# Kernel optimization log

Measured on AMD Instinct MI355X. Metric: run time of the kernel, lower is better.

## Reference

```python
import jax, jax.numpy as jnp
import numpy as np

B, T, N, D = 32, 32, 64, 512
H, OUT = 64, 256


def setup_inputs() -> dict:
    key = jax.random.key(0)
    ks = jax.random.split(key, 7)
    return {
        "inputs": jax.random.normal(ks[0], (B, T, N, D), dtype=jnp.float32),
        "ue_w": jax.random.normal(ks[1], (H, D), dtype=jnp.float32) * (1.0 / np.sqrt(D)),
        "ue_b": jax.random.normal(ks[2], (H,), dtype=jnp.float32) * 0.02,
        "be": jnp.zeros((H,), dtype=jnp.float32),
        "w_w": jax.random.normal(ks[3], (1, H), dtype=jnp.float32) * (1.0 / np.sqrt(H)),
        "w_b": jax.random.normal(ks[4], (1,), dtype=jnp.float32) * 0.02,
        "fc1_w": jax.random.normal(ks[5], (OUT, D), dtype=jnp.float32) * (1.0 / np.sqrt(D)),
        "fc1_b": jax.random.normal(ks[6], (OUT,), dtype=jnp.float32) * 0.02,
    }


def reference(inputs, ue_w, ue_b, be, w_w, w_b, fc1_w, fc1_b):
    # Train path of STAttn.
    b, t, n, d = inputs.shape
    x = inputs.reshape(b * t, n, d)                       # flatten(start=0, end=1)
    h = jnp.einsum('bnd,hd->bnh', x, ue_w) + ue_b + be    # ue(x) + be
    h = jax.nn.leaky_relu(h, negative_slope=0.2)
    e = jnp.einsum('bnh,oh->bno', h, w_w) + w_b           # [BT, N, 1] scores
    a = jax.nn.softmax(e, axis=-2)                        # softmax over N
    attr = jnp.sum(a * x, axis=1)                         # weighted pooling -> [BT, D]
    fc = attr @ fc1_w.T + fc1_b                           # [BT, 256]
    return fc.reshape(b, t, fc.shape[-1]).transpose(1, 0, 2)  # [T, B, 256]
```

## Files before the change

### kernel.cpp

```cpp
#include <hip/hip_runtime.h>


typedef __attribute__((ext_vector_type(8)))  short bf16x8;
typedef __attribute__((ext_vector_type(16))) float f32x16;

#define AS3(p) ((__attribute__((address_space(3))) void*)(p))
#define AS1(p) ((const __attribute__((address_space(1))) void*)(p))
#define WAITVM0() asm volatile("s_waitcnt vmcnt(0)" ::: "memory")
#define SCHEDB()  __builtin_amdgcn_sched_barrier(0)

__device__ __forceinline__ void split8t(const float* __restrict__ v,
                                        bf16x8& h8, bf16x8& l8) {
#pragma unroll
    for (int i = 0; i < 8; ++i) {
        const unsigned u = __float_as_uint(v[i]);
        h8[i] = (short)(u >> 16);
        const float hf = __uint_as_float(u & 0xFFFF0000u);
        l8[i] = (short)(__float_as_uint(v[i] - hf) >> 16);
    }
}

template<int MODE>
__global__ __launch_bounds__(512, 4) void stattn_main(
    const float* __restrict__ inp,
    const float* __restrict__ ue_w,
    const float* __restrict__ ue_b,
    const float* __restrict__ be,
    const float* __restrict__ w_w,
    const float* __restrict__ fc1_w,
    const float* __restrict__ fc1_b,
    float* __restrict__ dst)
{
    __shared__ __align__(16) float xb[2][64 * 64];
    __shared__ __align__(16) float wb[2][64 * 64];
    __shared__ float ep_s[2][64];
    __shared__ float a_s[64];
    __shared__ __align__(16) float attr_s[512];

    const int tid = threadIdx.x;
    const int wv  = tid >> 6;
    const int l   = tid & 63;
    const int l31 = l & 31;
    const int hi5 = l >> 5;
    const int kh  = wv & 1;
    const int jh  = (wv >> 1) & 1;
    const int nh  = wv >> 2;
    const float* __restrict__ xg = inp + (size_t)blockIdx.x * (64 * 512);

    const int r_a  = wv * 8 + (l >> 4);
    const int r_b  = r_a + 4;
    const int cph  = (l & 15) >> 1;
    const int hfl  = l & 1;
    const int colA = (cph ^ (r_a & 7)) * 8 + hfl * 4;
    const int colB = (cph ^ (r_b & 7)) * 8 + hfl * 4;
    const float* __restrict__ gxa = xg   + r_a * 512 + colA;
    const float* __restrict__ gxb = xg   + r_b * 512 + colB;
    const float* __restrict__ gwa = ue_w + r_a * 512 + colA;
    const float* __restrict__ gwb = ue_w + r_b * 512 + colB;

#define STAGE(buf, kt) do {                                                          \
    __builtin_amdgcn_global_load_lds(AS1(gxa + (kt) * 64),                           \
        AS3((char*)&xb[buf][0] + (wv * 8) * 256), 16, 0, 0);                         \
    __builtin_amdgcn_global_load_lds(AS1(gxb + (kt) * 64),                           \
        AS3((char*)&xb[buf][0] + (wv * 8 + 4) * 256), 16, 0, 0);                     \
    __builtin_amdgcn_global_load_lds(AS1(gwa + (kt) * 64),                           \
        AS3((char*)&wb[buf][0] + (wv * 8) * 256), 16, 0, 0);                         \
    __builtin_amdgcn_global_load_lds(AS1(gwb + (kt) * 64),                           \
        AS3((char*)&wb[buf][0] + (wv * 8 + 4) * 256), 16, 0, 0);                     \
} while (0)

    f32x16 acc = {};
    STAGE(0, 0);

    const int arow = nh * 32 + l31;
    const int brow = jh * 32 + l31;

#pragma unroll
    for (int kt = 0; kt < 8; ++kt) {
        const int cur = kt & 1;
        WAITVM0();
        SCHEDB();
        __builtin_amdgcn_s_barrier();
        SCHEDB();
        if (kt < 7) STAGE(cur ^ 1, kt + 1);
        const float* __restrict__ xrow = &xb[cur][arow * 64];
        const float* __restrict__ wrow = &wb[cur][brow * 64];
#pragma unroll
        for (int s = 0; s < 2; ++s) {
            const int ck = kh * 4 + 2 * s + hi5;
            const int pa = (ck ^ (arow & 7)) * 8;
            const int pb = (ck ^ (brow & 7)) * 8;
            float av[8], bv[8];
            *reinterpret_cast<float4*>(&av[0]) = *reinterpret_cast<const float4*>(&xrow[pa]);
            *reinterpret_cast<float4*>(&av[4]) = *reinterpret_cast<const float4*>(&xrow[pa + 4]);
            *reinterpret_cast<float4*>(&bv[0]) = *reinterpret_cast<const float4*>(&wrow[pb]);
            *reinterpret_cast<float4*>(&bv[4]) = *reinterpret_cast<const float4*>(&wrow[pb + 4]);
            bf16x8 ah, al, bh, bl;
            split8t(av, ah, al);
            split8t(bv, bh, bl);
            acc = __builtin_amdgcn_mfma_f32_32x32x16_bf16(ah, bh, acc, 0, 0, 0);
            acc = __builtin_amdgcn_mfma_f32_32x32x16_bf16(al, bh, acc, 0, 0, 0);
            acc = __builtin_amdgcn_mfma_f32_32x32x16_bf16(ah, bl, acc, 0, 0, 0);
        }
    }

    __syncthreads();
    {
        float* hp = &xb[0][0];
        const int toff = (nh * 2 + jh) * 1024 + l;
        if (kh == 1) {
#pragma unroll
            for (int r = 0; r < 16; ++r) hp[toff + r * 64] = acc[r];
        }
        __syncthreads();
        if (kh == 0) {
#pragma unroll
            for (int r = 0; r < 16; ++r) acc[r] += hp[toff + r * 64];
            const int j = jh * 32 + l31;
            const float bias = ue_b[j] + be[j];
            const float ww   = w_w[j];
#pragma unroll
            for (int r = 0; r < 16; ++r) {
                float hv = acc[r] + bias;
                hv = hv > 0.f ? hv : 0.2f * hv;
                float p = hv * ww;
                p += __shfl_xor(p, 1);
                p += __shfl_xor(p, 2);
                p += __shfl_xor(p, 4);
                p += __shfl_xor(p, 8);
                p += __shfl_xor(p, 16);
                if (l31 == 0) {
                    const int nr = (r & 3) + 8 * (r >> 2) + 4 * hi5;
                    ep_s[jh][nh * 32 + nr] = p;
                }
            }
        }
    }
    __syncthreads();

    {
        const float v = ep_s[0][l] + ep_s[1][l];
        float mx = v;
#pragma unroll
        for (int off = 32; off >= 1; off >>= 1) mx = fmaxf(mx, __shfl_xor(mx, off));
        const float ex = expf(v - mx);
        float sm = ex;
#pragma unroll
        for (int off = 32; off >= 1; off >>= 1) sm += __shfl_xor(sm, off);
        if (wv == 0) a_s[l] = ex / sm;
    }
    __syncthreads();

    {
        const int d = tid;
        float s = 0.f;
#pragma unroll 8
        for (int n = 0; n < 64; ++n) s = fmaf(a_s[n], xg[n * 512 + d], s);
        if (MODE == 0) {
            dst[(size_t)blockIdx.x * 512 + d] = s;
        } else {
            attr_s[d] = s;
        }
    }

    if (MODE == 1) {
        __syncthreads();
        const int o  = tid >> 1;
        const int ks = tid & 1;
        const float* __restrict__ wr = fc1_w + o * 512 + ks * 256;
        const float* __restrict__ ap = attr_s + ks * 256;
        float s0 = 0.f, s1 = 0.f, s2 = 0.f, s3 = 0.f;
#pragma unroll 8
        for (int i = 0; i < 64; ++i) {
            const float4 w4 = *reinterpret_cast<const float4*>(&wr[i * 4]);
            const float4 a4 = *reinterpret_cast<const float4*>(&ap[i * 4]);
            s0 = fmaf(a4.x, w4.x, s0);
            s1 = fmaf(a4.y, w4.y, s1);
            s2 = fmaf(a4.z, w4.z, s2);
            s3 = fmaf(a4.w, w4.w, s3);
        }
        float p = (s0 + s1) + (s2 + s3);
        p += __shfl_xor(p, 1);
        if (ks == 0) {
            const int bt  = blockIdx.x;
            const int row = (bt & 31) * 32 + (bt >> 5);
            dst[row * 256 + o] = p + fc1_b[o];
        }
    }
#undef STAGE
}

__global__ __launch_bounds__(256, 2) void stattn_fc2(
    const float* __restrict__ attr,
    const float* __restrict__ fc1_w,
    const float* __restrict__ fc1_b,
    float* __restrict__ out)
{
    __shared__ __align__(16) float at[32][516];
    const int tid = threadIdx.x;
    const int bm  = blockIdx.x;
    const int bn  = blockIdx.y;

    {
        const int row = tid >> 3;
        const int seg = tid & 7;
        const float* __restrict__ src = attr + (size_t)(bm * 32 + row) * 512 + seg * 64;
#pragma unroll
        for (int q = 0; q < 16; ++q)
            *reinterpret_cast<float4*>(&at[row][seg * 64 + q * 4]) =
                *reinterpret_cast<const float4*>(&src[q * 4]);
    }
    __syncthreads();

    const int tx = tid & 31;
    const int ty = tid >> 5;
    const int o  = bn * 32 + tx;
    const float* __restrict__ wr = fc1_w + (size_t)o * 512;
    float s0 = 0.f, s1 = 0.f, s2 = 0.f, s3 = 0.f;
#pragma unroll 4
    for (int kq = 0; kq < 128; ++kq) {
        const float4 w4 = *reinterpret_cast<const float4*>(&wr[kq * 4]);
        const float4 a0 = *reinterpret_cast<const float4*>(&at[ty * 4 + 0][kq * 4]);
        const float4 a1 = *reinterpret_cast<const float4*>(&at[ty * 4 + 1][kq * 4]);
        const float4 a2 = *reinterpret_cast<const float4*>(&at[ty * 4 + 2][kq * 4]);
        const float4 a3 = *reinterpret_cast<const float4*>(&at[ty * 4 + 3][kq * 4]);
        s0 += a0.x * w4.x + a0.y * w4.y + a0.z * w4.z + a0.w * w4.w;
        s1 += a1.x * w4.x + a1.y * w4.y + a1.z * w4.z + a1.w * w4.w;
        s2 += a2.x * w4.x + a2.y * w4.y + a2.z * w4.z + a2.w * w4.w;
        s3 += a3.x * w4.x + a3.y * w4.y + a3.z * w4.z + a3.w * w4.w;
    }
    const float fb = fc1_b[o];
    float sv[4] = {s0, s1, s2, s3};
#pragma unroll
    for (int j = 0; j < 4; ++j) {
        const int bt  = bm * 32 + ty * 4 + j;
        const int row = (bt & 31) * 32 + (bt >> 5);
        out[row * 256 + o] = sv[j] + fb;
    }
}

extern "C" void kernel_launch(void* const* d_in, const int* in_sizes, int n_in,
                              void* d_out, int out_size, void* d_ws, size_t ws_size,
                              hipStream_t stream) {
    const float* inp   = (const float*)d_in[0];
    const float* ue_w  = (const float*)d_in[1];
    const float* ue_b  = (const float*)d_in[2];
    const float* be    = (const float*)d_in[3];
    const float* w_w   = (const float*)d_in[4];
    const float* fc1_w = (const float*)d_in[6];
    const float* fc1_b = (const float*)d_in[7];
    float* out = (float*)d_out;

    const bool split = ws_size >= (size_t)1024 * 512 * 4;
    if (split) {
        float* attr = (float*)d_ws;
        stattn_main<0><<<1024, 512, 0, stream>>>(inp, ue_w, ue_b, be, w_w,
                                                 fc1_w, fc1_b, attr);
        stattn_fc2<<<dim3(32, 8), 256, 0, stream>>>(attr, fc1_w, fc1_b, out);
    } else {
        stattn_main<1><<<1024, 512, 0, stream>>>(inp, ue_w, ue_b, be, w_w,
                                                 fc1_w, fc1_b, out);
    }
}
```

Baseline: 74.30 us.

## Process two tokens per block with direct global MFMA operand loads, drop LDS staging

Each 512-thread block now handles two BT slices. Each group of four waves computes a full-K 64x64 score tile, reading MFMA operands directly from global memory instead of through double-buffered LDS with async global-to-LDS loads. This removes the split-K partial-sum exchange, the per-stage barriers and most of the LDS footprint, which allows higher occupancy. The cost is uncoalesced per-lane strided global reads with no software pipelining and L2 reuse only for ue_w. The pooling step also switches to float2 loads, and the launch now uses half as many blocks.

```diff
diff --git a/kernel.cpp b/kernel.cpp
--- a/kernel.cpp
+++ b/kernel.cpp
@@ -3,11 +3,6 @@
 
 typedef __attribute__((ext_vector_type(8)))  short bf16x8;
 typedef __attribute__((ext_vector_type(16))) float f32x16;
-
-#define AS3(p) ((__attribute__((address_space(3))) void*)(p))
-#define AS1(p) ((const __attribute__((address_space(1))) void*)(p))
-#define WAITVM0() asm volatile("s_waitcnt vmcnt(0)" ::: "memory")
-#define SCHEDB()  __builtin_amdgcn_sched_barrier(0)
 
 __device__ __forceinline__ void split8t(const float* __restrict__ v,
                                         bf16x8& h8, bf16x8& l8) {
@@ -31,115 +26,72 @@
     const float* __restrict__ fc1_b,
     float* __restrict__ dst)
 {
-    __shared__ __align__(16) float xb[2][64 * 64];
-    __shared__ __align__(16) float wb[2][64 * 64];
-    __shared__ float ep_s[2][64];
-    __shared__ float a_s[64];
-    __shared__ __align__(16) float attr_s[512];
+    __shared__ float ep_s[2][2][64];
+    __shared__ float a_s[2][64];
+    __shared__ __align__(16) float attr_s[2][512];
 
     const int tid = threadIdx.x;
     const int wv  = tid >> 6;
     const int l   = tid & 63;
     const int l31 = l & 31;
     const int hi5 = l >> 5;
-    const int kh  = wv & 1;
-    const int jh  = (wv >> 1) & 1;
-    const int nh  = wv >> 2;
-    const float* __restrict__ xg = inp + (size_t)blockIdx.x * (64 * 512);
-
-    const int r_a  = wv * 8 + (l >> 4);
-    const int r_b  = r_a + 4;
-    const int cph  = (l & 15) >> 1;
-    const int hfl  = l & 1;
-    const int colA = (cph ^ (r_a & 7)) * 8 + hfl * 4;
-    const int colB = (cph ^ (r_b & 7)) * 8 + hfl * 4;
-    const float* __restrict__ gxa = xg   + r_a * 512 + colA;
-    const float* __restrict__ gxb = xg   + r_b * 512 + colB;
-    const float* __restrict__ gwa = ue_w + r_a * 512 + colA;
-    const float* __restrict__ gwb = ue_w + r_b * 512 + colB;
-
-#define STAGE(buf, kt) do {                                                          \
-    __builtin_amdgcn_global_load_lds(AS1(gxa + (kt) * 64),                           \
-        AS3((char*)&xb[buf][0] + (wv * 8) * 256), 16, 0, 0);                         \
-    __builtin_amdgcn_global_load_lds(AS1(gxb + (kt) * 64),                           \
-        AS3((char*)&xb[buf][0] + (wv * 8 + 4) * 256), 16, 0, 0);                     \
-    __builtin_amdgcn_global_load_lds(AS1(gwa + (kt) * 64),                           \
-        AS3((char*)&wb[buf][0] + (wv * 8) * 256), 16, 0, 0);                         \
-    __builtin_amdgcn_global_load_lds(AS1(gwb + (kt) * 64),                           \
-        AS3((char*)&wb[buf][0] + (wv * 8 + 4) * 256), 16, 0, 0);                     \
-} while (0)
+    const int g   = wv >> 2;
+    const int nh  = (wv >> 1) & 1;
+    const int jh  = wv & 1;
+    const int kq  = hi5 * 8;
+
+    const long bt = (long)blockIdx.x * 2 + g;
+    const float* __restrict__ xg = inp + bt * (64 * 512);
+
+    const float* __restrict__ arow = xg   + (nh * 32 + l31) * 512 + kq;
+    const float* __restrict__ brow = ue_w + (jh * 32 + l31) * 512 + kq;
 
     f32x16 acc = {};
-    STAGE(0, 0);
-
-    const int arow = nh * 32 + l31;
-    const int brow = jh * 32 + l31;
-
-#pragma unroll
-    for (int kt = 0; kt < 8; ++kt) {
-        const int cur = kt & 1;
-        WAITVM0();
-        SCHEDB();
-        __builtin_amdgcn_s_barrier();
-        SCHEDB();
-        if (kt < 7) STAGE(cur ^ 1, kt + 1);
-        const float* __restrict__ xrow = &xb[cur][arow * 64];
-        const float* __restrict__ wrow = &wb[cur][brow * 64];
-#pragma unroll
-        for (int s = 0; s < 2; ++s) {
-            const int ck = kh * 4 + 2 * s + hi5;
-            const int pa = (ck ^ (arow & 7)) * 8;
-            const int pb = (ck ^ (brow & 7)) * 8;
-            float av[8], bv[8];
-            *reinterpret_cast<float4*>(&av[0]) = *reinterpret_cast<const float4*>(&xrow[pa]);
-            *reinterpret_cast<float4*>(&av[4]) = *reinterpret_cast<const float4*>(&xrow[pa + 4]);
-            *reinterpret_cast<float4*>(&bv[0]) = *reinterpret_cast<const float4*>(&wrow[pb]);
-            *reinterpret_cast<float4*>(&bv[4]) = *reinterpret_cast<const float4*>(&wrow[pb + 4]);
-            bf16x8 ah, al, bh, bl;
-            split8t(av, ah, al);
-            split8t(bv, bh, bl);
-            acc = __builtin_amdgcn_mfma_f32_32x32x16_bf16(ah, bh, acc, 0, 0, 0);
-            acc = __builtin_amdgcn_mfma_f32_32x32x16_bf16(al, bh, acc, 0, 0, 0);
-            acc = __builtin_amdgcn_mfma_f32_32x32x16_bf16(ah, bl, acc, 0, 0, 0);
-        }
-    }
-
+#pragma unroll 4
+    for (int ks = 0; ks < 32; ++ks) {
+        const int k = ks * 16;
+        float av[8], bv[8];
+        *reinterpret_cast<float4*>(&av[0]) = *reinterpret_cast<const float4*>(&arow[k]);
+        *reinterpret_cast<float4*>(&av[4]) = *reinterpret_cast<const float4*>(&arow[k + 4]);
+        *reinterpret_cast<float4*>(&bv[0]) = *reinterpret_cast<const float4*>(&brow[k]);
+        *reinterpret_cast<float4*>(&bv[4]) = *reinterpret_cast<const float4*>(&brow[k + 4]);
+        bf16x8 ah, al, bh, bl;
+        split8t(av, ah, al);
+        split8t(bv, bh, bl);
+        acc = __builtin_amdgcn_mfma_f32_32x32x16_bf16(ah, bh, acc, 0, 0, 0);
+        acc = __builtin_amdgcn_mfma_f32_32x32x16_bf16(al, bh, acc, 0, 0, 0);
+        acc = __builtin_amdgcn_mfma_f32_32x32x16_bf16(ah, bl, acc, 0, 0, 0);
+    }
+
+    {
+        const int j = jh * 32 + l31;
+        const float bias = ue_b[j] + be[j];
+        const float ww   = w_w[j];
+        float ep[16];
+#pragma unroll
+        for (int r = 0; r < 16; ++r) {
+            float hv = acc[r] + bias;
+            hv = hv > 0.f ? hv : 0.2f * hv;
+            float p = hv * ww;
+            p += __shfl_xor(p, 1);
+            p += __shfl_xor(p, 2);
+            p += __shfl_xor(p, 4);
+            p += __shfl_xor(p, 8);
+            p += __shfl_xor(p, 16);
+            ep[r] = p;
+        }
+        if (l31 == 0) {
+#pragma unroll
+            for (int r = 0; r < 16; ++r) {
+                const int nr = (r & 3) + 8 * (r >> 2) + 4 * hi5;
+                ep_s[g][jh][nh * 32 + nr] = ep[r];
+            }
+        }
+    }
     __syncthreads();
-    {
-        float* hp = &xb[0][0];
-        const int toff = (nh * 2 + jh) * 1024 + l;
-        if (kh == 1) {
-#pragma unroll
-            for (int r = 0; r < 16; ++r) hp[toff + r * 64] = acc[r];
-        }
-        __syncthreads();
-        if (kh == 0) {
-#pragma unroll
-            for (int r = 0; r < 16; ++r) acc[r] += hp[toff + r * 64];
-            const int j = jh * 32 + l31;
-            const float bias = ue_b[j] + be[j];
-            const float ww   = w_w[j];
-#pragma unroll
-            for (int r = 0; r < 16; ++r) {
-                float hv = acc[r] + bias;
-                hv = hv > 0.f ? hv : 0.2f * hv;
-                float p = hv * ww;
-                p += __shfl_xor(p, 1);
-                p += __shfl_xor(p, 2);
-                p += __shfl_xor(p, 4);
-                p += __shfl_xor(p, 8);
-                p += __shfl_xor(p, 16);
-                if (l31 == 0) {
-                    const int nr = (r & 3) + 8 * (r >> 2) + 4 * hi5;
-                    ep_s[jh][nh * 32 + nr] = p;
-                }
-            }
-        }
-    }
-    __syncthreads();
-
-    {
-        const float v = ep_s[0][l] + ep_s[1][l];
+
+    {
+        float v  = ep_s[g][0][l] + ep_s[g][1][l];
         float mx = v;
 #pragma unroll
         for (int off = 32; off >= 1; off >>= 1) mx = fmaxf(mx, __shfl_xor(mx, off));
@@ -147,31 +99,42 @@
         float sm = ex;
 #pragma unroll
         for (int off = 32; off >= 1; off >>= 1) sm += __shfl_xor(sm, off);
-        if (wv == 0) a_s[l] = ex / sm;
+        if ((wv & 3) == 0) a_s[g][l] = ex / sm;
     }
     __syncthreads();
 
     {
-        const int d = tid;
-        float s = 0.f;
+        const int gg = tid >> 8;
+        const int d0 = (tid & 255) * 2;
+        const float* __restrict__ xp =
+            inp + ((long)blockIdx.x * 2 + gg) * (64 * 512) + d0;
+        float ax = 0.f, ay = 0.f;
 #pragma unroll 8
-        for (int n = 0; n < 64; ++n) s = fmaf(a_s[n], xg[n * 512 + d], s);
+        for (int n = 0; n < 64; ++n) {
+            const float an  = a_s[gg][n];
+            const float2 xv = *reinterpret_cast<const float2*>(&xp[n * 512]);
+            ax = fmaf(an, xv.x, ax);
+            ay = fmaf(an, xv.y, ay);
+        }
         if (MODE == 0) {
-            dst[(size_t)blockIdx.x * 512 + d] = s;
+            float2 o; o.x = ax; o.y = ay;
+            *reinterpret_cast<float2*>(
+                &dst[((long)blockIdx.x * 2 + gg) * 512 + d0]) = o;
         } else {
-            attr_s[d] = s;
+            attr_s[gg][d0]     = ax;
+            attr_s[gg][d0 + 1] = ay;
         }
     }
 
     if (MODE == 1) {
         __syncthreads();
-        const int o  = tid >> 1;
-        const int ks = tid & 1;
-        const float* __restrict__ wr = fc1_w + o * 512 + ks * 256;
-        const float* __restrict__ ap = attr_s + ks * 256;
+        const int gg = tid >> 8;
+        const int o  = tid & 255;
+        const float* __restrict__ wr = fc1_w + o * 512;
+        const float* __restrict__ ap = attr_s[gg];
         float s0 = 0.f, s1 = 0.f, s2 = 0.f, s3 = 0.f;
 #pragma unroll 8
-        for (int i = 0; i < 64; ++i) {
+        for (int i = 0; i < 128; ++i) {
             const float4 w4 = *reinterpret_cast<const float4*>(&wr[i * 4]);
             const float4 a4 = *reinterpret_cast<const float4*>(&ap[i * 4]);
             s0 = fmaf(a4.x, w4.x, s0);
@@ -179,15 +142,10 @@
             s2 = fmaf(a4.z, w4.z, s2);
             s3 = fmaf(a4.w, w4.w, s3);
         }
-        float p = (s0 + s1) + (s2 + s3);
-        p += __shfl_xor(p, 1);
-        if (ks == 0) {
-            const int bt  = blockIdx.x;
-            const int row = (bt & 31) * 32 + (bt >> 5);
-            dst[row * 256 + o] = p + fc1_b[o];
-        }
-    }
-#undef STAGE
+        const long btg = (long)blockIdx.x * 2 + gg;
+        const int row  = (int)(btg & 31) * 32 + (int)(btg >> 5);
+        dst[row * 256 + o] = (s0 + s1) + (s2 + s3) + fc1_b[o];
+    }
 }
 
 __global__ __launch_bounds__(256, 2) void stattn_fc2(
@@ -254,11 +212,11 @@
     const bool split = ws_size >= (size_t)1024 * 512 * 4;
     if (split) {
         float* attr = (float*)d_ws;
-        stattn_main<0><<<1024, 512, 0, stream>>>(inp, ue_w, ue_b, be, w_w,
-                                                 fc1_w, fc1_b, attr);
+        stattn_main<0><<<512, 512, 0, stream>>>(inp, ue_w, ue_b, be, w_w,
+                                                fc1_w, fc1_b, attr);
         stattn_fc2<<<dim3(32, 8), 256, 0, stream>>>(attr, fc1_w, fc1_b, out);
     } else {
-        stattn_main<1><<<1024, 512, 0, stream>>>(inp, ue_w, ue_b, be, w_w,
-                                                 fc1_w, fc1_b, out);
-    }
-}
+        stattn_main<1><<<512, 512, 0, stream>>>(inp, ue_w, ue_b, be, w_w,
+                                                fc1_w, fc1_b, out);
+    }
+}
```

Result: slower. 97.55 us (+31.3%).

## Triple-buffer input tiles and load ue_w directly into registers

Applied to the files above, without the earlier changes.

The x tiles now go through a three-deep LDS ring with two tiles in flight, waiting with vmcnt(2) instead of draining all loads every iteration. The ue_w operand is no longer staged through LDS. Each lane loads its B fragment straight from global memory into registers, prefetched one k-step ahead. The launch bound drops from 4 to 2 blocks per SM, which frees registers at the risk of lower occupancy, and the direct weight loads rely on L2 hits and may be less coalesced.

```diff
diff --git a/kernel.cpp b/kernel.cpp
--- a/kernel.cpp
+++ b/kernel.cpp
@@ -6,8 +6,7 @@
 
 #define AS3(p) ((__attribute__((address_space(3))) void*)(p))
 #define AS1(p) ((const __attribute__((address_space(1))) void*)(p))
-#define WAITVM0() asm volatile("s_waitcnt vmcnt(0)" ::: "memory")
-#define SCHEDB()  __builtin_amdgcn_sched_barrier(0)
+#define SCHEDB() __builtin_amdgcn_sched_barrier(0)
 
 __device__ __forceinline__ void split8t(const float* __restrict__ v,
                                         bf16x8& h8, bf16x8& l8) {
@@ -21,7 +20,7 @@
 }
 
 template<int MODE>
-__global__ __launch_bounds__(512, 4) void stattn_main(
+__global__ __launch_bounds__(512, 2) void stattn_main(
     const float* __restrict__ inp,
     const float* __restrict__ ue_w,
     const float* __restrict__ ue_b,
@@ -31,8 +30,7 @@
     const float* __restrict__ fc1_b,
     float* __restrict__ dst)
 {
-    __shared__ __align__(16) float xb[2][64 * 64];
-    __shared__ __align__(16) float wb[2][64 * 64];
+    __shared__ __align__(16) float ring[3][64][64];
     __shared__ float ep_s[2][64];
     __shared__ float a_s[64];
     __shared__ __align__(16) float attr_s[512];
@@ -53,60 +51,82 @@
     const int hfl  = l & 1;
     const int colA = (cph ^ (r_a & 7)) * 8 + hfl * 4;
     const int colB = (cph ^ (r_b & 7)) * 8 + hfl * 4;
-    const float* __restrict__ gxa = xg   + r_a * 512 + colA;
-    const float* __restrict__ gxb = xg   + r_b * 512 + colB;
-    const float* __restrict__ gwa = ue_w + r_a * 512 + colA;
-    const float* __restrict__ gwb = ue_w + r_b * 512 + colB;
-
-#define STAGE(buf, kt) do {                                                          \
-    __builtin_amdgcn_global_load_lds(AS1(gxa + (kt) * 64),                           \
-        AS3((char*)&xb[buf][0] + (wv * 8) * 256), 16, 0, 0);                         \
-    __builtin_amdgcn_global_load_lds(AS1(gxb + (kt) * 64),                           \
-        AS3((char*)&xb[buf][0] + (wv * 8 + 4) * 256), 16, 0, 0);                     \
-    __builtin_amdgcn_global_load_lds(AS1(gwa + (kt) * 64),                           \
-        AS3((char*)&wb[buf][0] + (wv * 8) * 256), 16, 0, 0);                         \
-    __builtin_amdgcn_global_load_lds(AS1(gwb + (kt) * 64),                           \
-        AS3((char*)&wb[buf][0] + (wv * 8 + 4) * 256), 16, 0, 0);                     \
+    const float* __restrict__ gxa = xg + r_a * 512 + colA;
+    const float* __restrict__ gxb = xg + r_b * 512 + colB;
+
+#define STAGE(t_) do {                                                        \
+    __builtin_amdgcn_global_load_lds(AS1(gxa + (t_) * 64),                    \
+        AS3((char*)&ring[(t_) % 3][wv * 8][0]), 16, 0, 0);                    \
+    __builtin_amdgcn_global_load_lds(AS1(gxb + (t_) * 64),                    \
+        AS3((char*)&ring[(t_) % 3][wv * 8 + 4][0]), 16, 0, 0);                \
 } while (0)
 
+    const int arow = nh * 32 + l31;
+    const float* __restrict__ brow = ue_w + (jh * 32 + l31) * 512;
+    const int bc0 = (kh * 4 + 0 + hi5) * 8;
+    const int bc1 = (kh * 4 + 2 + hi5) * 8;
+    const int pa0 = ((kh * 4 + 0 + hi5) ^ (arow & 7)) * 8;
+    const int pa1 = ((kh * 4 + 2 + hi5) ^ (arow & 7)) * 8;
+
     f32x16 acc = {};
-    STAGE(0, 0);
-
-    const int arow = nh * 32 + l31;
-    const int brow = jh * 32 + l31;
-
-#pragma unroll
-    for (int kt = 0; kt < 8; ++kt) {
-        const int cur = kt & 1;
-        WAITVM0();
+    float4 bA0, bA1, bA2, bA3;
+
+    bA0 = *reinterpret_cast<const float4*>(&brow[bc0]);
+    bA1 = *reinterpret_cast<const float4*>(&brow[bc0 + 4]);
+    bA2 = *reinterpret_cast<const float4*>(&brow[bc1]);
+    bA3 = *reinterpret_cast<const float4*>(&brow[bc1 + 4]);
+    SCHEDB();
+    STAGE(0);
+    STAGE(1);
+    SCHEDB();
+
+#pragma unroll
+    for (int t = 0; t < 8; ++t) {
+        if (t < 7) asm volatile("s_waitcnt vmcnt(2)" ::: "memory");
+        else       asm volatile("s_waitcnt vmcnt(0)" ::: "memory");
         SCHEDB();
         __builtin_amdgcn_s_barrier();
         SCHEDB();
-        if (kt < 7) STAGE(cur ^ 1, kt + 1);
-        const float* __restrict__ xrow = &xb[cur][arow * 64];
-        const float* __restrict__ wrow = &wb[cur][brow * 64];
-#pragma unroll
-        for (int s = 0; s < 2; ++s) {
-            const int ck = kh * 4 + 2 * s + hi5;
-            const int pa = (ck ^ (arow & 7)) * 8;
-            const int pb = (ck ^ (brow & 7)) * 8;
+        float4 bn0, bn1, bn2, bn3;
+        if (t < 7) {
+            const float* __restrict__ bp = brow + (t + 1) * 64;
+            bn0 = *reinterpret_cast<const float4*>(&bp[bc0]);
+            bn1 = *reinterpret_cast<const float4*>(&bp[bc0 + 4]);
+            bn2 = *reinterpret_cast<const float4*>(&bp[bc1]);
+            bn3 = *reinterpret_cast<const float4*>(&bp[bc1 + 4]);
+        }
+        SCHEDB();
+        if (t < 6) STAGE(t + 2);
+        SCHEDB();
+        {
+            const float* __restrict__ rrow = &ring[t % 3][arow][0];
             float av[8], bv[8];
-            *reinterpret_cast<float4*>(&av[0]) = *reinterpret_cast<const float4*>(&xrow[pa]);
-            *reinterpret_cast<float4*>(&av[4]) = *reinterpret_cast<const float4*>(&xrow[pa + 4]);
-            *reinterpret_cast<float4*>(&bv[0]) = *reinterpret_cast<const float4*>(&wrow[pb]);
-            *reinterpret_cast<float4*>(&bv[4]) = *reinterpret_cast<const float4*>(&wrow[pb + 4]);
             bf16x8 ah, al, bh, bl;
+            *reinterpret_cast<float4*>(&av[0]) = *reinterpret_cast<const float4*>(&rrow[pa0]);
+            *reinterpret_cast<float4*>(&av[4]) = *reinterpret_cast<const float4*>(&rrow[pa0 + 4]);
+            *reinterpret_cast<float4*>(&bv[0]) = bA0;
+            *reinterpret_cast<float4*>(&bv[4]) = bA1;
             split8t(av, ah, al);
             split8t(bv, bh, bl);
             acc = __builtin_amdgcn_mfma_f32_32x32x16_bf16(ah, bh, acc, 0, 0, 0);
             acc = __builtin_amdgcn_mfma_f32_32x32x16_bf16(al, bh, acc, 0, 0, 0);
             acc = __builtin_amdgcn_mfma_f32_32x32x16_bf16(ah, bl, acc, 0, 0, 0);
-        }
-    }
-
-    __syncthreads();
-    {
-        float* hp = &xb[0][0];
+            *reinterpret_cast<float4*>(&av[0]) = *reinterpret_cast<const float4*>(&rrow[pa1]);
+            *reinterpret_cast<float4*>(&av[4]) = *reinterpret_cast<const float4*>(&rrow[pa1 + 4]);
+            *reinterpret_cast<float4*>(&bv[0]) = bA2;
+            *reinterpret_cast<float4*>(&bv[4]) = bA3;
+            split8t(av, ah, al);
+            split8t(bv, bh, bl);
+            acc = __builtin_amdgcn_mfma_f32_32x32x16_bf16(ah, bh, acc, 0, 0, 0);
+            acc = __builtin_amdgcn_mfma_f32_32x32x16_bf16(al, bh, acc, 0, 0, 0);
+            acc = __builtin_amdgcn_mfma_f32_32x32x16_bf16(ah, bl, acc, 0, 0, 0);
+        }
+        bA0 = bn0; bA1 = bn1; bA2 = bn2; bA3 = bn3;
+    }
+
+    __syncthreads();
+    {
+        float* hp = &ring[0][0][0];
         const int toff = (nh * 2 + jh) * 1024 + l;
         if (kh == 1) {
 #pragma unroll
```

Result: slower. 79.36 us (+6.8%).

## Keep whole x tile resident in LDS, preload weights to registers, reuse for pooling

Applied to the files above, without the earlier changes.

Loads the entire 64x512 input tile for a block into LDS up front, issuing all async global-to-LDS loads at once and waiting with decreasing vmcnt per k-tile instead of double-buffering. The ue_w B operand now goes straight into registers, so it no longer passes through LDS. The attention-weighted pooling reads x from LDS rather than re-reading global memory, using a per-wave partial sum followed by a cross-wave reduction. The cost is a much larger LDS footprint (128KB+) and 128 extra registers, with launch bounds lowered to 2 blocks per CU, which cuts occupancy.

```diff
diff --git a/kernel.cpp b/kernel.cpp
--- a/kernel.cpp
+++ b/kernel.cpp
@@ -6,8 +6,7 @@
 
 #define AS3(p) ((__attribute__((address_space(3))) void*)(p))
 #define AS1(p) ((const __attribute__((address_space(1))) void*)(p))
-#define WAITVM0() asm volatile("s_waitcnt vmcnt(0)" ::: "memory")
-#define SCHEDB()  __builtin_amdgcn_sched_barrier(0)
+#define SCHEDB() __builtin_amdgcn_sched_barrier(0)
 
 __device__ __forceinline__ void split8t(const float* __restrict__ v,
                                         bf16x8& h8, bf16x8& l8) {
@@ -21,7 +20,7 @@
 }
 
 template<int MODE>
-__global__ __launch_bounds__(512, 4) void stattn_main(
+__global__ __launch_bounds__(512, 2) void stattn_main(
     const float* __restrict__ inp,
     const float* __restrict__ ue_w,
     const float* __restrict__ ue_b,
@@ -31,11 +30,10 @@
     const float* __restrict__ fc1_b,
     float* __restrict__ dst)
 {
-    __shared__ __align__(16) float xb[2][64 * 64];
-    __shared__ __align__(16) float wb[2][64 * 64];
+    __shared__ __align__(16) float x_lds[8][64][64];
+    __shared__ __align__(16) float comb[4096];
     __shared__ float ep_s[2][64];
     __shared__ float a_s[64];
-    __shared__ __align__(16) float attr_s[512];
 
     const int tid = threadIdx.x;
     const int wv  = tid >> 6;
@@ -47,75 +45,84 @@
     const int nh  = wv >> 2;
     const float* __restrict__ xg = inp + (size_t)blockIdx.x * (64 * 512);
 
-    const int r_a  = wv * 8 + (l >> 4);
-    const int r_b  = r_a + 4;
-    const int cph  = (l & 15) >> 1;
-    const int hfl  = l & 1;
-    const int colA = (cph ^ (r_a & 7)) * 8 + hfl * 4;
-    const int colB = (cph ^ (r_b & 7)) * 8 + hfl * 4;
-    const float* __restrict__ gxa = xg   + r_a * 512 + colA;
-    const float* __restrict__ gxb = xg   + r_b * 512 + colB;
-    const float* __restrict__ gwa = ue_w + r_a * 512 + colA;
-    const float* __restrict__ gwb = ue_w + r_b * 512 + colB;
-
-#define STAGE(buf, kt) do {                                                          \
-    __builtin_amdgcn_global_load_lds(AS1(gxa + (kt) * 64),                           \
-        AS3((char*)&xb[buf][0] + (wv * 8) * 256), 16, 0, 0);                         \
-    __builtin_amdgcn_global_load_lds(AS1(gxb + (kt) * 64),                           \
-        AS3((char*)&xb[buf][0] + (wv * 8 + 4) * 256), 16, 0, 0);                     \
-    __builtin_amdgcn_global_load_lds(AS1(gwa + (kt) * 64),                           \
-        AS3((char*)&wb[buf][0] + (wv * 8) * 256), 16, 0, 0);                         \
-    __builtin_amdgcn_global_load_lds(AS1(gwb + (kt) * 64),                           \
-        AS3((char*)&wb[buf][0] + (wv * 8 + 4) * 256), 16, 0, 0);                     \
+    float bar[128];
+    {
+        const float* __restrict__ bp =
+            ue_w + (jh * 32 + l31) * 512 + kh * 32 + hi5 * 8;
+#pragma unroll
+        for (int t = 0; t < 8; ++t)
+#pragma unroll
+            for (int s = 0; s < 2; ++s) {
+                *reinterpret_cast<float4*>(&bar[(t * 2 + s) * 8]) =
+                    *reinterpret_cast<const float4*>(&bp[t * 64 + s * 16]);
+                *reinterpret_cast<float4*>(&bar[(t * 2 + s) * 8 + 4]) =
+                    *reinterpret_cast<const float4*>(&bp[t * 64 + s * 16 + 4]);
+            }
+    }
+    SCHEDB();
+
+    {
+        const int r0 = wv * 8 + (l >> 4);
+        const int r1 = r0 + 4;
+        const float* __restrict__ gx0 =
+            xg + r0 * 512 + 2 * (((l & 15) * 2) ^ (r0 & 30));
+        const float* __restrict__ gx1 =
+            xg + r1 * 512 + 2 * (((l & 15) * 2) ^ (r1 & 30));
+#pragma unroll
+        for (int t = 0; t < 8; ++t) {
+            __builtin_amdgcn_global_load_lds(AS1(gx0 + t * 64),
+                AS3(&x_lds[t][wv * 8][0]), 16, 0, 0);
+            __builtin_amdgcn_global_load_lds(AS1(gx1 + t * 64),
+                AS3(&x_lds[t][wv * 8 + 4][0]), 16, 0, 0);
+            SCHEDB();
+        }
+    }
+
+    f32x16 acc = {};
+    const int arow = nh * 32 + l31;
+    const int am   = arow & 30;
+
+#define KSTEP(T, S) do {                                                      \
+    float av[8];                                                              \
+    const int qb_ = kh * 16 + (S) * 8 + hi5 * 4;                              \
+    *reinterpret_cast<float2*>(&av[0]) = *reinterpret_cast<const float2*>(    \
+        &x_lds[T][arow][(((qb_ + 0) ^ am)) * 2]);                             \
+    *reinterpret_cast<float2*>(&av[2]) = *reinterpret_cast<const float2*>(    \
+        &x_lds[T][arow][(((qb_ + 1) ^ am)) * 2]);                             \
+    *reinterpret_cast<float2*>(&av[4]) = *reinterpret_cast<const float2*>(    \
+        &x_lds[T][arow][(((qb_ + 2) ^ am)) * 2]);                             \
+    *reinterpret_cast<float2*>(&av[6]) = *reinterpret_cast<const float2*>(    \
+        &x_lds[T][arow][(((qb_ + 3) ^ am)) * 2]);                             \
+    bf16x8 ah, al, bh, bl;                                                    \
+    split8t(av, ah, al);                                                      \
+    split8t(&bar[((T) * 2 + (S)) * 8], bh, bl);                               \
+    acc = __builtin_amdgcn_mfma_f32_32x32x16_bf16(ah, bh, acc, 0, 0, 0);      \
+    acc = __builtin_amdgcn_mfma_f32_32x32x16_bf16(al, bh, acc, 0, 0, 0);      \
+    acc = __builtin_amdgcn_mfma_f32_32x32x16_bf16(ah, bl, acc, 0, 0, 0);      \
 } while (0)
 
-    f32x16 acc = {};
-    STAGE(0, 0);
-
-    const int arow = nh * 32 + l31;
-    const int brow = jh * 32 + l31;
-
-#pragma unroll
-    for (int kt = 0; kt < 8; ++kt) {
-        const int cur = kt & 1;
-        WAITVM0();
-        SCHEDB();
-        __builtin_amdgcn_s_barrier();
-        SCHEDB();
-        if (kt < 7) STAGE(cur ^ 1, kt + 1);
-        const float* __restrict__ xrow = &xb[cur][arow * 64];
-        const float* __restrict__ wrow = &wb[cur][brow * 64];
-#pragma unroll
-        for (int s = 0; s < 2; ++s) {
-            const int ck = kh * 4 + 2 * s + hi5;
-            const int pa = (ck ^ (arow & 7)) * 8;
-            const int pb = (ck ^ (brow & 7)) * 8;
-            float av[8], bv[8];
-            *reinterpret_cast<float4*>(&av[0]) = *reinterpret_cast<const float4*>(&xrow[pa]);
-            *reinterpret_cast<float4*>(&av[4]) = *reinterpret_cast<const float4*>(&xrow[pa + 4]);
-            *reinterpret_cast<float4*>(&bv[0]) = *reinterpret_cast<const float4*>(&wrow[pb]);
-            *reinterpret_cast<float4*>(&bv[4]) = *reinterpret_cast<const float4*>(&wrow[pb + 4]);
-            bf16x8 ah, al, bh, bl;
-            split8t(av, ah, al);
-            split8t(bv, bh, bl);
-            acc = __builtin_amdgcn_mfma_f32_32x32x16_bf16(ah, bh, acc, 0, 0, 0);
-            acc = __builtin_amdgcn_mfma_f32_32x32x16_bf16(al, bh, acc, 0, 0, 0);
-            acc = __builtin_amdgcn_mfma_f32_32x32x16_bf16(ah, bl, acc, 0, 0, 0);
-        }
-    }
-
-    __syncthreads();
-    {
-        float* hp = &xb[0][0];
+#define TILE(T, VM) do {                                                      \
+    asm volatile("s_waitcnt vmcnt(" #VM ")" ::: "memory"); SCHEDB();          \
+    __builtin_amdgcn_s_barrier(); SCHEDB();                                   \
+    KSTEP(T, 0); KSTEP(T, 1);                                                 \
+} while (0)
+
+    TILE(0, 14); TILE(1, 12); TILE(2, 10); TILE(3, 8);
+    TILE(4, 6);  TILE(5, 4);  TILE(6, 2);  TILE(7, 0);
+#undef TILE
+#undef KSTEP
+
+    __syncthreads();
+    {
         const int toff = (nh * 2 + jh) * 1024 + l;
         if (kh == 1) {
 #pragma unroll
-            for (int r = 0; r < 16; ++r) hp[toff + r * 64] = acc[r];
+            for (int r = 0; r < 16; ++r) comb[toff + r * 64] = acc[r];
         }
         __syncthreads();
         if (kh == 0) {
 #pragma unroll
-            for (int r = 0; r < 16; ++r) acc[r] += hp[toff + r * 64];
+            for (int r = 0; r < 16; ++r) acc[r] += comb[toff + r * 64];
             const int j = jh * 32 + l31;
             const float bias = ue_b[j] + be[j];
             const float ww   = w_w[j];
@@ -152,14 +159,38 @@
     __syncthreads();
 
     {
+        float pa0 = 0.f, pa1 = 0.f, pa2 = 0.f, pa3 = 0.f;
+        float pb0 = 0.f, pb1 = 0.f, pb2 = 0.f, pb3 = 0.f;
+        const int t0 = l >> 4;
+        const int u0 = (2 * l) & 31;
+#pragma unroll
+        for (int n8 = 0; n8 < 8; ++n8) {
+            const int n  = wv * 8 + n8;
+            const float an = a_s[n];
+            const int ph = (u0 ^ (n & 30)) * 2;
+            const float4 v0 = *reinterpret_cast<const float4*>(&x_lds[t0][n][ph]);
+            const float4 v1 = *reinterpret_cast<const float4*>(&x_lds[t0 + 4][n][ph]);
+            pa0 = fmaf(an, v0.x, pa0); pa1 = fmaf(an, v0.y, pa1);
+            pa2 = fmaf(an, v0.z, pa2); pa3 = fmaf(an, v0.w, pa3);
+            pb0 = fmaf(an, v1.x, pb0); pb1 = fmaf(an, v1.y, pb1);
+            pb2 = fmaf(an, v1.z, pb2); pb3 = fmaf(an, v1.w, pb3);
+        }
+        float4 o0; o0.x = pa0; o0.y = pa1; o0.z = pa2; o0.w = pa3;
+        float4 o1; o1.x = pb0; o1.y = pb1; o1.z = pb2; o1.w = pb3;
+        *reinterpret_cast<float4*>(&comb[wv * 512 + 4 * l])       = o0;
+        *reinterpret_cast<float4*>(&comb[wv * 512 + 4 * l + 256]) = o1;
+    }
+    __syncthreads();
+
+    {
         const int d = tid;
         float s = 0.f;
-#pragma unroll 8
-        for (int n = 0; n < 64; ++n) s = fmaf(a_s[n], xg[n * 512 + d], s);
+#pragma unroll
+        for (int w = 0; w < 8; ++w) s += comb[w * 512 + d];
         if (MODE == 0) {
             dst[(size_t)blockIdx.x * 512 + d] = s;
         } else {
-            attr_s[d] = s;
+            reinterpret_cast<float*>(x_lds)[d] = s;
         }
     }
 
@@ -168,7 +199,7 @@
         const int o  = tid >> 1;
         const int ks = tid & 1;
         const float* __restrict__ wr = fc1_w + o * 512 + ks * 256;
-        const float* __restrict__ ap = attr_s + ks * 256;
+        const float* __restrict__ ap = reinterpret_cast<float*>(x_lds) + ks * 256;
         float s0 = 0.f, s1 = 0.f, s2 = 0.f, s3 = 0.f;
 #pragma unroll 8
         for (int i = 0; i < 64; ++i) {
@@ -187,7 +218,6 @@
             dst[row * 256 + o] = p + fc1_b[o];
         }
     }
-#undef STAGE
 }
 
 __global__ __launch_bounds__(256, 2) void stattn_fc2(
```

After: 95.50 us. 28.5% more time.
